# Performance work log

Hardware: AMD Instinct MI355X
Metric: run time of the kernel (lower is better)

The kernel has to match this reference:

```python
import math
import jax, jax.numpy as jnp
import numpy as np

B, T, D = 1, 4096, 1024
NH, NKV, HD = 16, 4, 64          # nhead, n_kv_heads, head_dim
WINDOW = 256


def _alibi_slopes(nhead: int) -> np.ndarray:
    closest_pow2 = 2 ** math.floor(math.log2(nhead))
    base = 2.0 ** (-2.0 ** (-(math.log2(closest_pow2) - 3)))
    slopes = base ** np.arange(1, closest_pow2 + 1, dtype=np.float32)
    if closest_pow2 < nhead:
        extra_base = 2.0 ** (-2.0 ** (-(math.log2(2 * closest_pow2) - 3)))
        extra = extra_base ** np.arange(1, 2 * (nhead - closest_pow2) + 1, 2, dtype=np.float32)
        slopes = np.concatenate([slopes, extra])
    return slopes.astype(np.float32)


def setup_inputs() -> dict:
    key = jax.random.key(0)
    ks = jax.random.split(key, 9)
    s = 0.02
    return {
        "x": jax.random.normal(ks[0], (B, T, D), jnp.float32),
        "Wq": jax.random.normal(ks[1], (D, NH * HD), jnp.float32) * s,
        "bq": jax.random.normal(ks[2], (NH * HD,), jnp.float32) * s,
        "Wk": jax.random.normal(ks[3], (D, NKV * HD), jnp.float32) * s,
        "bk": jax.random.normal(ks[4], (NKV * HD,), jnp.float32) * s,
        "Wv": jax.random.normal(ks[5], (D, NKV * HD), jnp.float32) * s,
        "bv": jax.random.normal(ks[6], (NKV * HD,), jnp.float32) * s,
        "Wo": jax.random.normal(ks[7], (D, D), jnp.float32) * s,
        "bo": jax.random.normal(ks[8], (D,), jnp.float32) * s,
    }


def _attn_bias():
    # ALiBi bias + causal + sliding-window mask, shape (NH, T, T)
    pos = jnp.arange(T)
    dist = pos[None, :] - pos[:, None]          # col - row; <=0 where causal-allowed
    allowed = (dist <= 0) & (-dist < WINDOW)    # causal AND within window
    slopes = jnp.asarray(_alibi_slopes(NH))     # (NH,)
    bias = -slopes[:, None, None] * jnp.abs(dist)[None].astype(jnp.float32)
    return jnp.where(allowed[None], bias, -jnp.inf)  # (NH, T, T)


def reference(x, Wq, bq, Wk, bk, Wv, bv, Wo, bo):
    q = (x @ Wq + bq).reshape(B, T, NH, HD).transpose(0, 2, 1, 3)   # (B,NH,T,HD)
    k = (x @ Wk + bk).reshape(B, T, NKV, HD).transpose(0, 2, 1, 3)  # (B,NKV,T,HD)
    v = (x @ Wv + bv).reshape(B, T, NKV, HD).transpose(0, 2, 1, 3)
    # GQA: repeat_interleave kv heads to NH
    k = jnp.repeat(k, NH // NKV, axis=1)
    v = jnp.repeat(v, NH // NKV, axis=1)
    scale = 1.0 / math.sqrt(HD)
    scores = jnp.einsum("bhtd,bhsd->bhts", q, k) * scale + _attn_bias()[None]
    probs = jax.nn.softmax(scores, axis=-1)
    out = jnp.einsum("bhts,bhsd->bhtd", probs, v)        # (B,NH,T,HD)
    out = out.transpose(0, 2, 1, 3).reshape(B, T, D)
    return out @ Wo + bo
```

## Files before the change

kernel.cpp:

```cpp
#include <hip/hip_runtime.h>

typedef __bf16 bf16;
typedef __bf16 bf16x8 __attribute__((ext_vector_type(8)));
typedef float f32x4 __attribute__((ext_vector_type(4)));

#define T_LEN   4096
#define D_MODEL 1024
#define QKV_LD  1536
#define VT_LD   4128
#define WINDOW  256


__global__ void cvt_f32_bf16(const float* __restrict__ in, bf16* __restrict__ out, int n) {
    int i = (blockIdx.x * blockDim.x + threadIdx.x) * 8;
    if (i >= n) return;
    float4 a = *(const float4*)(in + i);
    float4 b = *(const float4*)(in + i + 4);
    bf16x8 o;
    o[0] = (bf16)a.x; o[1] = (bf16)a.y; o[2] = (bf16)a.z; o[3] = (bf16)a.w;
    o[4] = (bf16)b.x; o[5] = (bf16)b.y; o[6] = (bf16)b.z; o[7] = (bf16)b.w;
    *(bf16x8*)(out + i) = o;
}

__global__ void concat_bias(const float* __restrict__ bq, const float* __restrict__ bk,
                            const float* __restrict__ bv, float* __restrict__ out) {
    int i = blockIdx.x * blockDim.x + threadIdx.x;
    if (i < 1024)      out[i] = bq[i];
    else if (i < 1280) out[i] = bk[i - 1024];
    else               out[i] = bv[i - 1280];
}

__global__ void transpose_w(const float* __restrict__ W, bf16* __restrict__ Wt, int K, int N) {
    __shared__ float t[32][33];
    int n0 = blockIdx.x * 32, k0 = blockIdx.y * 32;
    int tx = threadIdx.x & 31, ty = threadIdx.x >> 5;
#pragma unroll
    for (int it = 0; it < 4; ++it)
        t[ty + it * 8][tx] = W[(size_t)(k0 + ty + it * 8) * N + n0 + tx];
    __syncthreads();
#pragma unroll
    for (int it = 0; it < 4; ++it)
        Wt[(size_t)(n0 + ty + it * 8) * K + k0 + tx] = (bf16)t[tx][ty + it * 8];
}

__global__ void transpose_v(const bf16* __restrict__ QKV, bf16* __restrict__ Vt) {
    __shared__ bf16 t[32][33];
    int t0 = blockIdx.x * 32;
    int c0 = blockIdx.y * 32;
    int tx = threadIdx.x & 31, ty = threadIdx.x >> 5;
#pragma unroll
    for (int it = 0; it < 4; ++it)
        t[ty + it * 8][tx] = QKV[(size_t)(t0 + ty + it * 8) * QKV_LD + 1280 + c0 + tx];
    __syncthreads();
#pragma unroll
    for (int it = 0; it < 4; ++it)
        Vt[(size_t)(c0 + ty + it * 8) * VT_LD + t0 + tx] = t[tx][ty + it * 8];
}


template <bool OUT_BF16>
__global__ __launch_bounds__(256) void gemm_bt(
    const bf16* __restrict__ A, const bf16* __restrict__ Bt,
    const float* __restrict__ bias, void* __restrict__ Cv,
    int M, int N, int K)
{
    __shared__ bf16 As[128][40];
    __shared__ bf16 Bs[64][40];
    const int m0 = blockIdx.y * 128;
    const int n0 = blockIdx.x * 64;
    const int tid  = threadIdx.x;
    const int wave = tid >> 6, lane = tid & 63;
    const int quad = lane >> 4, l16 = lane & 15;
    const int wm = wave >> 1, wn = wave & 1;

    f32x4 acc[4][2] = {};

    const int arow = tid >> 1, ahalf = (tid & 1) * 16;
    const bf16* aptr = A + (size_t)(m0 + arow) * K + ahalf;
    const bf16* bptr = Bt + (size_t)(n0 + arow) * K + ahalf;

    const int nk = K >> 5;
    for (int kt = 0; kt < nk; ++kt) {
        uint4 av0 = *(const uint4*)(aptr + kt * 32);
        uint4 av1 = *(const uint4*)(aptr + kt * 32 + 8);
        uint4 bv0, bv1;
        if (tid < 128) {
            bv0 = *(const uint4*)(bptr + kt * 32);
            bv1 = *(const uint4*)(bptr + kt * 32 + 8);
        }
        __syncthreads();
        *(uint4*)&As[arow][ahalf]     = av0;
        *(uint4*)&As[arow][ahalf + 8] = av1;
        if (tid < 128) {
            *(uint4*)&Bs[arow][ahalf]     = bv0;
            *(uint4*)&Bs[arow][ahalf + 8] = bv1;
        }
        __syncthreads();
        bf16x8 af[4], bfr[2];
#pragma unroll
        for (int i = 0; i < 4; ++i)
            af[i] = *(const bf16x8*)&As[wm * 64 + i * 16 + l16][quad * 8];
#pragma unroll
        for (int j = 0; j < 2; ++j)
            bfr[j] = *(const bf16x8*)&Bs[wn * 32 + j * 16 + l16][quad * 8];
#pragma unroll
        for (int i = 0; i < 4; ++i)
#pragma unroll
            for (int j = 0; j < 2; ++j)
                acc[i][j] = __builtin_amdgcn_mfma_f32_16x16x32_bf16(af[i], bfr[j], acc[i][j], 0, 0, 0);
    }

#pragma unroll
    for (int i = 0; i < 4; ++i)
#pragma unroll
        for (int j = 0; j < 2; ++j) {
            const int col = n0 + wn * 32 + j * 16 + l16;
            const float bb = bias[col];
#pragma unroll
            for (int r = 0; r < 4; ++r) {
                const int row = m0 + wm * 64 + i * 16 + quad * 4 + r;
                const float v = acc[i][j][r] + bb;
                if (OUT_BF16) ((bf16*)Cv)[(size_t)row * N + col] = (bf16)v;
                else          ((float*)Cv)[(size_t)row * N + col] = v;
            }
        }
}


__global__ __launch_bounds__(64) void attn_kernel(
    const bf16* __restrict__ QKV, const bf16* __restrict__ Vt, bf16* __restrict__ Oa)
{
    __shared__ bf16 Ps[16][296];
    const int q0 = blockIdx.x * 16;
    const int h  = blockIdx.y;
    const int kh = h >> 2;
    const int lane = threadIdx.x;
    const int quad = lane >> 4, l16 = lane & 15;
    const float slope = exp2f(-0.5f * (float)(h + 1));
    const int lo = (q0 >= 256) ? (q0 - 256) : 0;

    const bf16* qp = QKV + (size_t)(q0 + l16) * QKV_LD + h * 64 + quad * 8;
    bf16x8 qf0 = *(const bf16x8*)qp;
    bf16x8 qf1 = *(const bf16x8*)(qp + 32);

    f32x4 s[17];
#pragma unroll
    for (int t = 0; t < 17; ++t) {
        const bf16* kp = QKV + (size_t)(lo + t * 16 + l16) * QKV_LD + D_MODEL + kh * 64 + quad * 8;
        bf16x8 kf0 = *(const bf16x8*)kp;
        bf16x8 kf1 = *(const bf16x8*)(kp + 32);
        f32x4 a = {};
        a = __builtin_amdgcn_mfma_f32_16x16x32_bf16(qf0, kf0, a, 0, 0, 0);
        a = __builtin_amdgcn_mfma_f32_16x16x32_bf16(qf1, kf1, a, 0, 0, 0);
        s[t] = a;
    }

    float rinv[4];
#pragma unroll
    for (int r = 0; r < 4; ++r) {
        const int row = q0 + quad * 4 + r;
        float mx = -1e30f;
#pragma unroll
        for (int t = 0; t < 17; ++t) {
            const int key = lo + t * 16 + l16;
            float v = s[t][r] * 0.125f - slope * (float)(row - key);
            const bool ok = (key <= row) && (key > row - WINDOW);
            v = ok ? v : -1e30f;
            s[t][r] = v;
            mx = fmaxf(mx, v);
        }
#pragma unroll
        for (int d = 1; d < 16; d <<= 1) mx = fmaxf(mx, __shfl_xor(mx, d));
        float sum = 0.f;
#pragma unroll
        for (int t = 0; t < 17; ++t) {
            float p = __expf(s[t][r] - mx);
            s[t][r] = p;
            sum += p;
        }
#pragma unroll
        for (int d = 1; d < 16; d <<= 1) sum += __shfl_xor(sum, d);
        rinv[r] = 1.f / sum;
    }

    {
        int idx = lane;
#pragma unroll
        for (int it = 0; it < 4; ++it) {
            Ps[(idx >> 4) & 15][272 + (idx & 15)] = (bf16)0.f;
            idx += 64;
        }
    }
#pragma unroll
    for (int t = 0; t < 17; ++t)
#pragma unroll
        for (int r = 0; r < 4; ++r)
            Ps[quad * 4 + r][t * 16 + l16] = (bf16)(s[t][r] * rinv[r]);
    __syncthreads();

    f32x4 o[4] = {};
#pragma unroll
    for (int c = 0; c < 9; ++c) {
        bf16x8 pf = *(const bf16x8*)&Ps[l16][c * 32 + quad * 8];
#pragma unroll
        for (int j = 0; j < 4; ++j) {
            const bf16* vp = Vt + (size_t)(kh * 64 + j * 16 + l16) * VT_LD + lo + c * 32 + quad * 8;
            bf16x8 vf = *(const bf16x8*)vp;
            o[j] = __builtin_amdgcn_mfma_f32_16x16x32_bf16(pf, vf, o[j], 0, 0, 0);
        }
    }

#pragma unroll
    for (int j = 0; j < 4; ++j)
#pragma unroll
        for (int r = 0; r < 4; ++r)
            Oa[(size_t)(q0 + quad * 4 + r) * D_MODEL + h * 64 + j * 16 + l16] = (bf16)o[j][r];
}


extern "C" void kernel_launch(void* const* d_in, const int* in_sizes, int n_in,
                              void* d_out, int out_size, void* d_ws, size_t ws_size,
                              hipStream_t stream) {
    const float* x  = (const float*)d_in[0];
    const float* Wq = (const float*)d_in[1];
    const float* bq = (const float*)d_in[2];
    const float* Wk = (const float*)d_in[3];
    const float* bk = (const float*)d_in[4];
    const float* Wv = (const float*)d_in[5];
    const float* bv = (const float*)d_in[6];
    const float* Wo = (const float*)d_in[7];
    const float* bo = (const float*)d_in[8];
    float* out = (float*)d_out;

    char* ws = (char*)d_ws;
    bf16*  xb    = (bf16*)(ws);
    bf16*  WtQKV = (bf16*)(ws + 8388608);
    bf16*  WtO   = (bf16*)(ws + 11534336);
    float* biasQ = (float*)(ws + 13631488);
    bf16*  QKV   = (bf16*)(ws + 13637632);
    bf16*  Vt    = (bf16*)(ws + 26220544);
    bf16*  AO    = (bf16*)(ws + 28334080);

    cvt_f32_bf16<<<2048, 256, 0, stream>>>(x, xb, 4096 * 1024);
    concat_bias<<<6, 256, 0, stream>>>(bq, bk, bv, biasQ);
    transpose_w<<<dim3(32, 32), 256, 0, stream>>>(Wq, WtQKV, 1024, 1024);
    transpose_w<<<dim3(8, 32), 256, 0, stream>>>(Wk, WtQKV + (size_t)1024 * 1024, 1024, 256);
    transpose_w<<<dim3(8, 32), 256, 0, stream>>>(Wv, WtQKV + (size_t)1280 * 1024, 1024, 256);
    transpose_w<<<dim3(32, 32), 256, 0, stream>>>(Wo, WtO, 1024, 1024);

    gemm_bt<true><<<dim3(24, 32), 256, 0, stream>>>(xb, WtQKV, biasQ, QKV, 4096, 1536, 1024);
    transpose_v<<<dim3(128, 8), 256, 0, stream>>>(QKV, Vt);
    attn_kernel<<<dim3(256, 16), 64, 0, stream>>>(QKV, Vt, AO);
    gemm_bt<false><<<dim3(16, 32), 256, 0, stream>>>(AO, WtO, bo, out, 4096, 1024, 1024);
}
```

Measured before the change: 188.2 us.

## Use direct global-to-LDS loads and 128x128 tiles in GEMM, merge QKV weight transposes

The GEMM kernel now stages A and B tiles straight into LDS with global_load_lds instead of going through registers. The N tile grows from 64 to 128, so each wave computes a 64x64 output block with 16 accumulators, which raises data reuse per load. The three Q/K/V weight transposes are merged into one launch. The unpadded LDS layout (row stride 32 bf16) may cause bank conflicts on fragment reads. The larger tiles also halve the block count (384 and 256 blocks on a 256-CU device), which lowers occupancy and may leave wave-quantization imbalance.

```diff
diff --git a/kernel.cpp b/kernel.cpp
--- a/kernel.cpp
+++ b/kernel.cpp
@@ -9,6 +9,11 @@
 #define QKV_LD  1536
 #define VT_LD   4128
 #define WINDOW  256
+
+__device__ __forceinline__ void gload_lds16(const bf16* g, bf16* l) {
+    __builtin_amdgcn_global_load_lds((const __attribute__((address_space(1))) void*)g,
+                                     (__attribute__((address_space(3))) void*)l, 16, 0, 0);
+}
 
 
 __global__ void cvt_f32_bf16(const float* __restrict__ in, bf16* __restrict__ out, int n) {
@@ -30,6 +35,24 @@
     else               out[i] = bv[i - 1280];
 }
 
+__global__ void transpose_wqkv(const float* __restrict__ Wq, const float* __restrict__ Wk,
+                               const float* __restrict__ Wv, bf16* __restrict__ Wt) {
+    __shared__ float t[32][33];
+    int n0 = blockIdx.x * 32, k0 = blockIdx.y * 32;
+    const float* W; int Ns, nofs;
+    if (n0 < 1024)      { W = Wq; Ns = 1024; nofs = 0; }
+    else if (n0 < 1280) { W = Wk; Ns = 256;  nofs = 1024; }
+    else                { W = Wv; Ns = 256;  nofs = 1280; }
+    int tx = threadIdx.x & 31, ty = threadIdx.x >> 5;
+#pragma unroll
+    for (int it = 0; it < 4; ++it)
+        t[ty + it * 8][tx] = W[(size_t)(k0 + ty + it * 8) * Ns + (n0 - nofs) + tx];
+    __syncthreads();
+#pragma unroll
+    for (int it = 0; it < 4; ++it)
+        Wt[(size_t)(n0 + ty + it * 8) * 1024 + k0 + tx] = (bf16)t[tx][ty + it * 8];
+}
+
 __global__ void transpose_w(const float* __restrict__ W, bf16* __restrict__ Wt, int K, int N) {
     __shared__ float t[32][33];
     int n0 = blockIdx.x * 32, k0 = blockIdx.y * 32;
@@ -64,57 +87,55 @@
     const float* __restrict__ bias, void* __restrict__ Cv,
     int M, int N, int K)
 {
-    __shared__ bf16 As[128][40];
-    __shared__ bf16 Bs[64][40];
+    __shared__ bf16 As[128 * 32];
+    __shared__ bf16 Bs[128 * 32];
     const int m0 = blockIdx.y * 128;
-    const int n0 = blockIdx.x * 64;
+    const int n0 = blockIdx.x * 128;
     const int tid  = threadIdx.x;
     const int wave = tid >> 6, lane = tid & 63;
     const int quad = lane >> 4, l16 = lane & 15;
     const int wm = wave >> 1, wn = wave & 1;
 
-    f32x4 acc[4][2] = {};
-
-    const int arow = tid >> 1, ahalf = (tid & 1) * 16;
-    const bf16* aptr = A + (size_t)(m0 + arow) * K + ahalf;
-    const bf16* bptr = Bt + (size_t)(n0 + arow) * K + ahalf;
+    f32x4 acc[4][4] = {};
+
+    const int srow = wave * 32 + (lane >> 2);
+    const int scol = (lane & 3) * 8;
+    const bf16* ga0 = A  + (size_t)(m0 + srow) * K + scol;
+    const bf16* ga1 = A  + (size_t)(m0 + srow + 16) * K + scol;
+    const bf16* gb0 = Bt + (size_t)(n0 + srow) * K + scol;
+    const bf16* gb1 = Bt + (size_t)(n0 + srow + 16) * K + scol;
+    bf16* la0 = As + srow * 32 + scol;
+    bf16* la1 = As + (srow + 16) * 32 + scol;
+    bf16* lb0 = Bs + srow * 32 + scol;
+    bf16* lb1 = Bs + (srow + 16) * 32 + scol;
 
     const int nk = K >> 5;
     for (int kt = 0; kt < nk; ++kt) {
-        uint4 av0 = *(const uint4*)(aptr + kt * 32);
-        uint4 av1 = *(const uint4*)(aptr + kt * 32 + 8);
-        uint4 bv0, bv1;
-        if (tid < 128) {
-            bv0 = *(const uint4*)(bptr + kt * 32);
-            bv1 = *(const uint4*)(bptr + kt * 32 + 8);
-        }
         __syncthreads();
-        *(uint4*)&As[arow][ahalf]     = av0;
-        *(uint4*)&As[arow][ahalf + 8] = av1;
-        if (tid < 128) {
-            *(uint4*)&Bs[arow][ahalf]     = bv0;
-            *(uint4*)&Bs[arow][ahalf + 8] = bv1;
-        }
+        gload_lds16(ga0 + kt * 32, la0);
+        gload_lds16(ga1 + kt * 32, la1);
+        gload_lds16(gb0 + kt * 32, lb0);
+        gload_lds16(gb1 + kt * 32, lb1);
         __syncthreads();
-        bf16x8 af[4], bfr[2];
+        bf16x8 af[4], bfr[4];
 #pragma unroll
         for (int i = 0; i < 4; ++i)
-            af[i] = *(const bf16x8*)&As[wm * 64 + i * 16 + l16][quad * 8];
-#pragma unroll
-        for (int j = 0; j < 2; ++j)
-            bfr[j] = *(const bf16x8*)&Bs[wn * 32 + j * 16 + l16][quad * 8];
+            af[i] = *(const bf16x8*)&As[(wm * 64 + i * 16 + l16) * 32 + quad * 8];
+#pragma unroll
+        for (int j = 0; j < 4; ++j)
+            bfr[j] = *(const bf16x8*)&Bs[(wn * 64 + j * 16 + l16) * 32 + quad * 8];
 #pragma unroll
         for (int i = 0; i < 4; ++i)
 #pragma unroll
-            for (int j = 0; j < 2; ++j)
+            for (int j = 0; j < 4; ++j)
                 acc[i][j] = __builtin_amdgcn_mfma_f32_16x16x32_bf16(af[i], bfr[j], acc[i][j], 0, 0, 0);
     }
 
 #pragma unroll
     for (int i = 0; i < 4; ++i)
 #pragma unroll
-        for (int j = 0; j < 2; ++j) {
-            const int col = n0 + wn * 32 + j * 16 + l16;
+        for (int j = 0; j < 4; ++j) {
+            const int col = n0 + wn * 64 + j * 16 + l16;
             const float bb = bias[col];
 #pragma unroll
             for (int r = 0; r < 4; ++r) {
@@ -243,13 +264,11 @@
 
     cvt_f32_bf16<<<2048, 256, 0, stream>>>(x, xb, 4096 * 1024);
     concat_bias<<<6, 256, 0, stream>>>(bq, bk, bv, biasQ);
-    transpose_w<<<dim3(32, 32), 256, 0, stream>>>(Wq, WtQKV, 1024, 1024);
-    transpose_w<<<dim3(8, 32), 256, 0, stream>>>(Wk, WtQKV + (size_t)1024 * 1024, 1024, 256);
-    transpose_w<<<dim3(8, 32), 256, 0, stream>>>(Wv, WtQKV + (size_t)1280 * 1024, 1024, 256);
+    transpose_wqkv<<<dim3(48, 32), 256, 0, stream>>>(Wq, Wk, Wv, WtQKV);
     transpose_w<<<dim3(32, 32), 256, 0, stream>>>(Wo, WtO, 1024, 1024);
 
-    gemm_bt<true><<<dim3(24, 32), 256, 0, stream>>>(xb, WtQKV, biasQ, QKV, 4096, 1536, 1024);
+    gemm_bt<true><<<dim3(12, 32), 256, 0, stream>>>(xb, WtQKV, biasQ, QKV, 4096, 1536, 1024);
     transpose_v<<<dim3(128, 8), 256, 0, stream>>>(QKV, Vt);
     attn_kernel<<<dim3(256, 16), 64, 0, stream>>>(QKV, Vt, AO);
-    gemm_bt<false><<<dim3(16, 32), 256, 0, stream>>>(AO, WtO, bo, out, 4096, 1024, 1024);
-}
+    gemm_bt<false><<<dim3(8, 32), 256, 0, stream>>>(AO, WtO, bo, out, 4096, 1024, 1024);
+}
```

Result: no change. 188.5 us (+0.2%).
